# Kernel tuning notes

Measured on AMD Instinct MI355X. Metric: run time of the kernel, lower is better.

Reference implementation:

```python
import jax, jax.numpy as jnp
import numpy as np
from jax import lax

B, C, H, W = 32, 256, 64, 64
MCH = 16   # max(8, 256//16)
KS = 5     # ECA 1D kernel: int((log2(256)+1)/2)=4 -> odd-adjust 5
EPS = 1e-5

def setup_inputs() -> dict:
    key = jax.random.key(0)
    ks = jax.random.split(key, 9)
    return {
        "x": jax.random.normal(ks[0], (B, C, H, W), jnp.float32),
        "w10": jax.random.normal(ks[1], (MCH, C), jnp.float32) * 0.05,   # 1x1 conv C->MCH
        "w11": jax.random.normal(ks[2], (C, MCH), jnp.float32) * 0.05,   # 1x1 conv MCH->C
        "bn_gamma": jax.random.normal(ks[3], (MCH,), jnp.float32) * 0.1 + 1.0,
        "bn_beta": jax.random.normal(ks[4], (MCH,), jnp.float32) * 0.1,
        "bn_mean": jax.random.normal(ks[5], (MCH,), jnp.float32) * 0.1,
        "bn_var": jax.random.uniform(ks[6], (MCH,), jnp.float32, 0.5, 1.5),
        "w20": jax.random.normal(ks[7], (KS,), jnp.float32) * 0.2,       # 1D ECA kernel
        "w21": jax.random.normal(ks[8], (1, 1, 3, 3), jnp.float32) * 0.2,  # spatial 3x3
    }

def reference(x, w10, w11, bn_gamma, bn_beta, bn_mean, bn_var, w20, w21):
    b, c, h, w = x.shape
    # --- channel (ECA) branch: global avg pool -> 1D conv over channel dim ---
    pooled = jnp.mean(x, axis=(2, 3))                      # [b, c]
    f_ch = lax.conv_general_dilated(
        pooled[:, None, :], w20[None, None, :], (1,), 'SAME',
        dimension_numbers=('NCH', 'OIH', 'NCH'))[:, 0, :]   # [b, c]
    f_ch = f_ch[:, :, None, None]                           # [b, c, 1, 1] (no sigmoid, as in source)
    # --- spatial branch: channel mean -> 3x3 conv -> sigmoid ---
    f_sa = jax.nn.sigmoid(lax.conv_general_dilated(
        jnp.mean(x, axis=1, keepdims=True), w21, (1, 1), 'SAME',
        dimension_numbers=('NCHW', 'OIHW', 'NCHW')))        # [b, 1, h, w]
    # --- coordinate branch ---
    x_h = jnp.mean(x, axis=3)                               # [b, c, h]
    x_w = jnp.mean(x, axis=2)                               # [b, c, w]
    cat = jnp.concatenate([x_h, x_w], axis=2)               # [b, c, h+w]
    y = jnp.einsum('mc,bcl->bml', w10, cat)                 # 1x1 conv
    inv = lax.rsqrt(bn_var + EPS) * bn_gamma                # BN (inference)
    y = jax.nn.relu(y * inv[None, :, None] + (bn_beta - bn_mean * inv)[None, :, None])
    yh, yw = y[:, :, :h], y[:, :, h:]
    s_h = jax.nn.sigmoid(jnp.einsum('cm,bmh->bch', w11, yh))[:, :, :, None]  # [b,c,h,1]
    s_w = jax.nn.sigmoid(jnp.einsum('cm,bmw->bcw', w11, yw))[:, :, None, :]  # [b,c,1,w]
    F = f_ch + s_h * s_w + f_sa
    return x * F
```

## Files before the change

### kernel.cpp

```cpp
#include <hip/hip_runtime.h>
#include <hip/hip_bf16.h>

#define NB 32
#define NC 256
#define NH 64
#define NW 64

typedef unsigned short u16;

__device__ int   g_mode;
__device__ float g_cmean[NB * 4096];
__device__ float g_catT[NB * 128 * NC];
__device__ float g_fch[NB * NC];
__device__ float g_fsa[NB * 4096];
__device__ float g_sh[NB * NC * 64];
__device__ float g_sw[NB * NC * 64];

__device__ __forceinline__ float bf2f(unsigned int u) {
    union { unsigned int i; float f; } v; v.i = u << 16; return v.f;
}
__device__ __forceinline__ u16 f2bf(float f) {
    union { float f; unsigned int i; } v; v.f = f;
    unsigned int i = v.i;
    unsigned int r = (i + 0x7fffu + ((i >> 16) & 1u)) >> 16;
    return (u16)r;
}
__device__ __forceinline__ float sigmoidf_(float x) {
    return 1.f / (1.f + expf(-x));
}

__device__ __forceinline__ void loadx8(const void* x, size_t i8, int mode, float* v) {
    if (mode) {
        const uint4 u = ((const uint4*)x)[i8];
        v[0] = bf2f(u.x & 0xffffu); v[1] = bf2f(u.x >> 16);
        v[2] = bf2f(u.y & 0xffffu); v[3] = bf2f(u.y >> 16);
        v[4] = bf2f(u.z & 0xffffu); v[5] = bf2f(u.z >> 16);
        v[6] = bf2f(u.w & 0xffffu); v[7] = bf2f(u.w >> 16);
    } else {
        const float4 a = ((const float4*)x)[i8 * 2];
        const float4 b = ((const float4*)x)[i8 * 2 + 1];
        v[0] = a.x; v[1] = a.y; v[2] = a.z; v[3] = a.w;
        v[4] = b.x; v[5] = b.y; v[6] = b.z; v[7] = b.w;
    }
}
__device__ __forceinline__ float loadw(const void* p, int i, int mode) {
    return mode ? bf2f((unsigned int)((const u16*)p)[i]) : ((const float*)p)[i];
}
__device__ __forceinline__ void store8(void* o, size_t i8, int mode, const float* v) {
    if (mode) {
        uint4 u;
        u.x = (unsigned int)f2bf(v[0]) | ((unsigned int)f2bf(v[1]) << 16);
        u.y = (unsigned int)f2bf(v[2]) | ((unsigned int)f2bf(v[3]) << 16);
        u.z = (unsigned int)f2bf(v[4]) | ((unsigned int)f2bf(v[5]) << 16);
        u.w = (unsigned int)f2bf(v[6]) | ((unsigned int)f2bf(v[7]) << 16);
        ((uint4*)o)[i8] = u;
    } else {
        ((float4*)o)[i8 * 2]     = make_float4(v[0], v[1], v[2], v[3]);
        ((float4*)o)[i8 * 2 + 1] = make_float4(v[4], v[5], v[6], v[7]);
    }
}

__global__ __launch_bounds__(256) void kSniff(const u16* __restrict__ xr) {
    __shared__ int cnt;
    if (threadIdx.x == 0) cnt = 0;
    __syncthreads();
    int local = 0;
#pragma unroll
    for (int i = 0; i < 8; ++i) {
        const u16 w = xr[(threadIdx.x * 8 + i) * 2];
        const unsigned e = (w >> 7) & 0xffu;
        if (w == 0 || (e >= 0x40u && e <= 0x90u)) ++local;
    }
    atomicAdd(&cnt, local);
    __syncthreads();
    if (threadIdx.x == 0) g_mode = (cnt >= 1536) ? 1 : 0;
}

__global__ __launch_bounds__(256) void kZero() {
    const int j = (blockIdx.x * 256 + threadIdx.x) * 4;
    *(float4*)(g_cmean + j) = make_float4(0.f, 0.f, 0.f, 0.f);
}

__global__ __launch_bounds__(256) void kA(const void* __restrict__ x) {
    __shared__ float cmean_lds[4096];
    __shared__ __align__(16) float plane_f[4096];
    __shared__ float rowsum[16 * 64];
    __shared__ float colsum[16 * 64];
    __shared__ float colpart[256];

    const int t  = threadIdx.x;
    const int cg = blockIdx.x;
    const int b  = blockIdx.y;
    const int mode = g_mode;

    for (int j = t; j < 4096; j += 256) cmean_lds[j] = 0.f;
    __syncthreads();

    for (int ch = 0; ch < 16; ++ch) {
        const int c = cg * 16 + ch;
        const size_t plane_i8 = ((size_t)(b * NC + c)) << 9;
#pragma unroll
        for (int i = 0; i < 2; ++i) {
            const int j = i * 2048 + t * 8;
            float v[8];
            loadx8(x, plane_i8 + (j >> 3), mode, v);
            *(float4*)(plane_f + j)     = make_float4(v[0], v[1], v[2], v[3]);
            *(float4*)(plane_f + j + 4) = make_float4(v[4], v[5], v[6], v[7]);
            cmean_lds[j + 0] += v[0]; cmean_lds[j + 1] += v[1];
            cmean_lds[j + 2] += v[2]; cmean_lds[j + 3] += v[3];
            cmean_lds[j + 4] += v[4]; cmean_lds[j + 5] += v[5];
            cmean_lds[j + 6] += v[6]; cmean_lds[j + 7] += v[7];
            float s = ((v[0] + v[1]) + (v[2] + v[3])) + ((v[4] + v[5]) + (v[6] + v[7]));
            s += __shfl_xor(s, 1);
            s += __shfl_xor(s, 2);
            s += __shfl_xor(s, 4);
            if ((t & 7) == 0) rowsum[ch * 64 + (j >> 6)] = s;
        }
        __syncthreads();
        {
            const int col = t & 63, hr = t >> 6;
            float p = 0.f;
#pragma unroll
            for (int hh = 0; hh < 16; ++hh)
                p += plane_f[(hr * 16 + hh) * 64 + col];
            colpart[t] = p;
        }
        __syncthreads();
        if (t < 64)
            colsum[ch * 64 + t] =
                colpart[t] + colpart[64 + t] + colpart[128 + t] + colpart[192 + t];
        __syncthreads();
    }

    const float inv64 = 1.f / 64.f;
    {
        const int lc = t & 15;
#pragma unroll
        for (int r = 0; r < 8; ++r) {
            const int l = r * 16 + (t >> 4);
            const float val =
                (l < 64 ? rowsum[lc * 64 + l] : colsum[lc * 64 + (l - 64)]) * inv64;
            g_catT[((size_t)(b * 128 + l)) * NC + cg * 16 + lc] = val;
        }
    }
    const float invC = 1.f / 256.f;
    for (int j = t; j < 4096; j += 256)
        atomicAdd(&g_cmean[b * 4096 + j], cmean_lds[j] * invC);
}

#define W10_STRIDE 260
__global__ __launch_bounds__(256) void kB(
    const void* __restrict__ w10, const void* __restrict__ w11,
    const void* __restrict__ bn_gamma, const void* __restrict__ bn_beta,
    const void* __restrict__ bn_mean, const void* __restrict__ bn_var,
    const void* __restrict__ w20, const void* __restrict__ w21) {

    __shared__ __align__(16) float un[48 * W10_STRIDE];
    __shared__ float y_lds[16 * 129];
    __shared__ float pooled[260];
    __shared__ float bnA[16], bnB[16], w20f[5], w21f[9];

    const int t = threadIdx.x, b = blockIdx.x;
    const int mode = g_mode;
    float* w10_lds = un;
    float* cat_lds = un + 16 * W10_STRIDE;

    for (int j = t; j < 4096; j += 256)
        w10_lds[(j >> 8) * W10_STRIDE + (j & 255)] = loadw(w10, j, mode);
    if (t < 16) {
        const float inv = rsqrtf(loadw(bn_var, t, mode) + 1e-5f) *
                          loadw(bn_gamma, t, mode);
        bnA[t] = inv;
        bnB[t] = loadw(bn_beta, t, mode) - loadw(bn_mean, t, mode) * inv;
    }
    if (t < 5) w20f[t] = loadw(w20, t, mode);
    if (t < 9) w21f[t] = loadw(w21, t, mode);
    {
        float p = 0.f;
        for (int l = 0; l < 64; ++l) p += g_catT[((size_t)(b * 128 + l)) * NC + t];
        pooled[2 + t] = p * (1.f / 64.f);
    }
    if (t < 2) { pooled[t] = 0.f; pooled[258 + t] = 0.f; }
    __syncthreads();
    {
        float acc = 0.f;
#pragma unroll
        for (int k = 0; k < 5; ++k) acc = fmaf(w20f[k], pooled[t + k], acc);
        g_fch[b * 256 + t] = acc;
    }
    for (int q = 0; q < 4; ++q) {
        __syncthreads();
#pragma unroll
        for (int r = 0; r < 8; ++r) {
            const int idx4 = r * 256 + t;
            const int l = idx4 >> 6;
            const int c = (idx4 & 63) << 2;
            const float4 v =
                *(const float4*)(g_catT + ((size_t)(b * 128 + q * 32 + l)) * NC + c);
            *(float4*)(cat_lds + l * W10_STRIDE + c) = v;
        }
        __syncthreads();
#pragma unroll
        for (int rep = 0; rep < 2; ++rep) {
            const int o = rep * 256 + t;
            const int m = o & 15, li = o >> 4;
            const float4* wr = (const float4*)(w10_lds + m * W10_STRIDE);
            const float4* cr = (const float4*)(cat_lds + li * W10_STRIDE);
            float acc = 0.f;
#pragma unroll 8
            for (int c4 = 0; c4 < 64; ++c4) {
                const float4 a = wr[c4], v = cr[c4];
                acc = fmaf(a.x, v.x, fmaf(a.y, v.y, fmaf(a.z, v.z, fmaf(a.w, v.w, acc))));
            }
            const float yv = fmaxf(fmaf(acc, bnA[m], bnB[m]), 0.f);
            y_lds[m * 129 + q * 32 + li] = yv;
        }
    }
    __syncthreads();
    float* w11f = un;
    float* cm   = un + 4096;
    for (int j = t; j < 4096; j += 256) {
        w11f[j] = loadw(w11, j, mode);
        cm[j]   = g_cmean[b * 4096 + j];
    }
    __syncthreads();
    for (int it = 0; it < 64; ++it) {
        const int c  = it * 4 + (t >> 6);
        const int hw = t & 63;
        const float* wc = w11f + c * 16;
        float ah = 0.f, aw = 0.f;
#pragma unroll
        for (int m = 0; m < 16; ++m) {
            ah = fmaf(wc[m], y_lds[m * 129 + hw], ah);
            aw = fmaf(wc[m], y_lds[m * 129 + 64 + hw], aw);
        }
        g_sh[((size_t)(b * NC + c)) * 64 + hw] = sigmoidf_(ah);
        g_sw[((size_t)(b * NC + c)) * 64 + hw] = sigmoidf_(aw);
    }
    for (int r = 0; r < 16; ++r) {
        const int j = r * 256 + t;
        const int h = j >> 6, w = j & 63;
        float acc = 0.f;
#pragma unroll
        for (int dy = 0; dy < 3; ++dy) {
            const int hy = h + dy - 1;
            if (hy < 0 || hy > 63) continue;
#pragma unroll
            for (int dx = 0; dx < 3; ++dx) {
                const int wx = w + dx - 1;
                if (wx < 0 || wx > 63) continue;
                acc = fmaf(w21f[dy * 3 + dx], cm[hy * 64 + wx], acc);
            }
        }
        g_fsa[b * 4096 + j] = sigmoidf_(acc);
    }
}

__global__ __launch_bounds__(256) void kC(const void* __restrict__ x,
                                          void* __restrict__ out) {
    const unsigned e = blockIdx.x * 256 + threadIdx.x;
    const int w0 = (e & 7) << 3;
    const int h  = (e >> 3) & 63;
    const int c  = (e >> 9) & 255;
    const int b  = e >> 17;
    const int mode = g_mode;

    float v[8];
    loadx8(x, e, mode, v);

    const float fc = g_fch[b * 256 + c];
    const float sh = g_sh[((size_t)(b * NC + c)) * 64 + h];
    const float* swp = g_sw + ((size_t)(b * NC + c)) * 64 + w0;
    const float* fsp = g_fsa + (size_t)b * 4096 + h * 64 + w0;
    const float4 swa = *(const float4*)(swp);
    const float4 swb = *(const float4*)(swp + 4);
    const float4 fsa = *(const float4*)(fsp);
    const float4 fsb = *(const float4*)(fsp + 4);

    float r[8];
    r[0] = v[0] * (fc + sh * swa.x + fsa.x);
    r[1] = v[1] * (fc + sh * swa.y + fsa.y);
    r[2] = v[2] * (fc + sh * swa.z + fsa.z);
    r[3] = v[3] * (fc + sh * swa.w + fsa.w);
    r[4] = v[4] * (fc + sh * swb.x + fsb.x);
    r[5] = v[5] * (fc + sh * swb.y + fsb.y);
    r[6] = v[6] * (fc + sh * swb.z + fsb.z);
    r[7] = v[7] * (fc + sh * swb.w + fsb.w);

    store8(out, e, mode, r);
}

extern "C" void kernel_launch(void* const* d_in, const int* in_sizes, int n_in,
                              void* d_out, int out_size, void* d_ws, size_t ws_size,
                              hipStream_t stream) {
    const void* x        = d_in[0];
    const void* w10      = d_in[1];
    const void* w11      = d_in[2];
    const void* bn_gamma = d_in[3];
    const void* bn_beta  = d_in[4];
    const void* bn_mean  = d_in[5];
    const void* bn_var   = d_in[6];
    const void* w20      = d_in[7];
    const void* w21      = d_in[8];

    kSniff<<<1, 256, 0, stream>>>((const u16*)x);
    kZero<<<(NB * 4096 / 4) / 256, 256, 0, stream>>>();
    kA<<<dim3(16, NB), 256, 0, stream>>>(x);
    kB<<<NB, 256, 0, stream>>>(w10, w11, bn_gamma, bn_beta,
                               bn_mean, bn_var, w20, w21);
    kC<<<(NB * NC * NH * NW / 8) / 256, 256, 0, stream>>>(x, d_out);
}
```

Before: 320.1 us.

## Restructure pooling kernel per-wave and split the coordinate kernel across blocks

In the pooling kernel, each wave now processes 4 channels and keeps column sums in registers, reducing them with shuffles. This removes the per-channel LDS plane staging and three block barriers per channel. Channel-mean partials are packed as bf16 in LDS and written to per-channel-group buffers instead of atomics, so the zeroing kernel can be dropped. The second kernel now runs 4 blocks per batch, splitting the h/w halves, the channel halves and the f_ch/f_sa side work, which adds parallelism. The cost is some duplicated weight loads and a small precision loss in the channel mean from the bf16 partials.

Result: no change. 313.8 us (-2.0%).

```diff
diff --git a/kernel.cpp b/kernel.cpp
--- a/kernel.cpp
+++ b/kernel.cpp
@@ -9,7 +9,7 @@
 typedef unsigned short u16;
 
 __device__ int   g_mode;
-__device__ float g_cmean[NB * 4096];
+__device__ float g_cmeanp[NB * 16 * 4096];
 __device__ float g_catT[NB * 128 * NC];
 __device__ float g_fch[NB * NC];
 __device__ float g_fsa[NB * 4096];
@@ -24,6 +24,9 @@
     unsigned int i = v.i;
     unsigned int r = (i + 0x7fffu + ((i >> 16) & 1u)) >> 16;
     return (u16)r;
+}
+__device__ __forceinline__ unsigned int pack2(float a, float b) {
+    return (unsigned int)f2bf(a) | ((unsigned int)f2bf(b) << 16);
 }
 __device__ __forceinline__ float sigmoidf_(float x) {
     return 1.f / (1.f + expf(-x));
@@ -49,10 +52,10 @@
 __device__ __forceinline__ void store8(void* o, size_t i8, int mode, const float* v) {
     if (mode) {
         uint4 u;
-        u.x = (unsigned int)f2bf(v[0]) | ((unsigned int)f2bf(v[1]) << 16);
-        u.y = (unsigned int)f2bf(v[2]) | ((unsigned int)f2bf(v[3]) << 16);
-        u.z = (unsigned int)f2bf(v[4]) | ((unsigned int)f2bf(v[5]) << 16);
-        u.w = (unsigned int)f2bf(v[6]) | ((unsigned int)f2bf(v[7]) << 16);
+        u.x = pack2(v[0], v[1]);
+        u.y = pack2(v[2], v[3]);
+        u.z = pack2(v[4], v[5]);
+        u.w = pack2(v[6], v[7]);
         ((uint4*)o)[i8] = u;
     } else {
         ((float4*)o)[i8 * 2]     = make_float4(v[0], v[1], v[2], v[3]);
@@ -76,61 +79,74 @@
     if (threadIdx.x == 0) g_mode = (cnt >= 1536) ? 1 : 0;
 }
 
-__global__ __launch_bounds__(256) void kZero() {
-    const int j = (blockIdx.x * 256 + threadIdx.x) * 4;
-    *(float4*)(g_cmean + j) = make_float4(0.f, 0.f, 0.f, 0.f);
-}
-
 __global__ __launch_bounds__(256) void kA(const void* __restrict__ x) {
-    __shared__ float cmean_lds[4096];
-    __shared__ __align__(16) float plane_f[4096];
+    __shared__ unsigned int sliceP[4][2048];
     __shared__ float rowsum[16 * 64];
     __shared__ float colsum[16 * 64];
-    __shared__ float colpart[256];
 
     const int t  = threadIdx.x;
+    const int ln = t & 63, wv = t >> 6;
     const int cg = blockIdx.x;
     const int b  = blockIdx.y;
     const int mode = g_mode;
 
-    for (int j = t; j < 4096; j += 256) cmean_lds[j] = 0.f;
-    __syncthreads();
-
-    for (int ch = 0; ch < 16; ++ch) {
-        const int c = cg * 16 + ch;
-        const size_t plane_i8 = ((size_t)(b * NC + c)) << 9;
-#pragma unroll
-        for (int i = 0; i < 2; ++i) {
-            const int j = i * 2048 + t * 8;
+    float colacc[4][8];
+#pragma unroll
+    for (int cc = 0; cc < 4; ++cc)
+#pragma unroll
+        for (int k = 0; k < 8; ++k) colacc[cc][k] = 0.f;
+
+    const int ch0 = cg * 16 + wv * 4;
+    const size_t i8base = (((size_t)(b * NC + ch0)) << 9) + ln;
+
+    for (int p = 0; p < 8; ++p) {
+        float cme[8];
+#pragma unroll
+        for (int k = 0; k < 8; ++k) cme[k] = 0.f;
+#pragma unroll
+        for (int cc = 0; cc < 4; ++cc) {
             float v[8];
-            loadx8(x, plane_i8 + (j >> 3), mode, v);
-            *(float4*)(plane_f + j)     = make_float4(v[0], v[1], v[2], v[3]);
-            *(float4*)(plane_f + j + 4) = make_float4(v[4], v[5], v[6], v[7]);
-            cmean_lds[j + 0] += v[0]; cmean_lds[j + 1] += v[1];
-            cmean_lds[j + 2] += v[2]; cmean_lds[j + 3] += v[3];
-            cmean_lds[j + 4] += v[4]; cmean_lds[j + 5] += v[5];
-            cmean_lds[j + 6] += v[6]; cmean_lds[j + 7] += v[7];
+            loadx8(x, i8base + (((size_t)cc) << 9) + p * 64, mode, v);
+#pragma unroll
+            for (int k = 0; k < 8; ++k) {
+                cme[k] += v[k];
+                colacc[cc][k] += v[k];
+            }
             float s = ((v[0] + v[1]) + (v[2] + v[3])) + ((v[4] + v[5]) + (v[6] + v[7]));
             s += __shfl_xor(s, 1);
             s += __shfl_xor(s, 2);
             s += __shfl_xor(s, 4);
-            if ((t & 7) == 0) rowsum[ch * 64 + (j >> 6)] = s;
-        }
-        __syncthreads();
-        {
-            const int col = t & 63, hr = t >> 6;
-            float p = 0.f;
-#pragma unroll
-            for (int hh = 0; hh < 16; ++hh)
-                p += plane_f[(hr * 16 + hh) * 64 + col];
-            colpart[t] = p;
-        }
-        __syncthreads();
-        if (t < 64)
-            colsum[ch * 64 + t] =
-                colpart[t] + colpart[64 + t] + colpart[128 + t] + colpart[192 + t];
-        __syncthreads();
-    }
+            if ((ln & 7) == 0)
+                rowsum[(wv * 4 + cc) * 64 + p * 8 + (ln >> 3)] = s;
+        }
+        uint4 pk;
+        pk.x = pack2(cme[0], cme[1]);
+        pk.y = pack2(cme[2], cme[3]);
+        pk.z = pack2(cme[4], cme[5]);
+        pk.w = pack2(cme[6], cme[7]);
+        *(uint4*)&sliceP[wv][p * 256 + ln * 4] = pk;
+    }
+
+#pragma unroll
+    for (int cc = 0; cc < 4; ++cc)
+#pragma unroll
+        for (int k = 0; k < 8; ++k) {
+            float v = colacc[cc][k];
+            v += __shfl_xor(v, 8);
+            v += __shfl_xor(v, 16);
+            v += __shfl_xor(v, 32);
+            colacc[cc][k] = v;
+        }
+    if (ln < 8) {
+#pragma unroll
+        for (int cc = 0; cc < 4; ++cc) {
+            *(float4*)&colsum[(wv * 4 + cc) * 64 + ln * 8] =
+                make_float4(colacc[cc][0], colacc[cc][1], colacc[cc][2], colacc[cc][3]);
+            *(float4*)&colsum[(wv * 4 + cc) * 64 + ln * 8 + 4] =
+                make_float4(colacc[cc][4], colacc[cc][5], colacc[cc][6], colacc[cc][7]);
+        }
+    }
+    __syncthreads();
 
     const float inv64 = 1.f / 64.f;
     {
@@ -143,116 +159,154 @@
             g_catT[((size_t)(b * 128 + l)) * NC + cg * 16 + lc] = val;
         }
     }
-    const float invC = 1.f / 256.f;
-    for (int j = t; j < 4096; j += 256)
-        atomicAdd(&g_cmean[b * 4096 + j], cmean_lds[j] * invC);
-}
-
-#define W10_STRIDE 260
+    {
+        const int u0 = t * 8;
+        float acc[16];
+#pragma unroll
+        for (int k = 0; k < 16; ++k) acc[k] = 0.f;
+#pragma unroll
+        for (int w = 0; w < 4; ++w) {
+            const uint4 qa = *(const uint4*)&sliceP[w][u0];
+            const uint4 qb = *(const uint4*)&sliceP[w][u0 + 4];
+            const unsigned int uu[8] = {qa.x, qa.y, qa.z, qa.w, qb.x, qb.y, qb.z, qb.w};
+#pragma unroll
+            for (int k = 0; k < 8; ++k) {
+                acc[2 * k]     += bf2f(uu[k] & 0xffffu);
+                acc[2 * k + 1] += bf2f(uu[k] >> 16);
+            }
+        }
+        const float invC = 1.f / 256.f;
+        float* dst = g_cmeanp + (((size_t)(b * 16 + cg)) << 12) + t * 16;
+#pragma unroll
+        for (int k4 = 0; k4 < 4; ++k4)
+            *(float4*)(dst + k4 * 4) = make_float4(acc[k4 * 4] * invC,
+                                                   acc[k4 * 4 + 1] * invC,
+                                                   acc[k4 * 4 + 2] * invC,
+                                                   acc[k4 * 4 + 3] * invC);
+    }
+}
+
 __global__ __launch_bounds__(256) void kB(
     const void* __restrict__ w10, const void* __restrict__ w11,
     const void* __restrict__ bn_gamma, const void* __restrict__ bn_beta,
     const void* __restrict__ bn_mean, const void* __restrict__ bn_var,
     const void* __restrict__ w20, const void* __restrict__ w21) {
 
-    __shared__ __align__(16) float un[48 * W10_STRIDE];
-    __shared__ float y_lds[16 * 129];
+    __shared__ float w10_lds[16 * 260];
+    __shared__ float w11_lds[2048];
+    __shared__ float y_lds[16 * 65];
+    __shared__ float cm[4096];
     __shared__ float pooled[260];
-    __shared__ float bnA[16], bnB[16], w20f[5], w21f[9];
-
-    const int t = threadIdx.x, b = blockIdx.x;
+    __shared__ float bnA[16], bnBv[16];
+
+    const int t  = threadIdx.x;
+    const int bx = blockIdx.x;
+    const int half = bx >> 1, csplit = bx & 1;
+    const int b  = blockIdx.y;
     const int mode = g_mode;
-    float* w10_lds = un;
-    float* cat_lds = un + 16 * W10_STRIDE;
 
     for (int j = t; j < 4096; j += 256)
-        w10_lds[(j >> 8) * W10_STRIDE + (j & 255)] = loadw(w10, j, mode);
+        w10_lds[(j >> 8) * 260 + (j & 255)] = loadw(w10, j, mode);
+    for (int j = t; j < 2048; j += 256)
+        w11_lds[j] = loadw(w11, csplit * 2048 + j, mode);
     if (t < 16) {
         const float inv = rsqrtf(loadw(bn_var, t, mode) + 1e-5f) *
                           loadw(bn_gamma, t, mode);
-        bnA[t] = inv;
-        bnB[t] = loadw(bn_beta, t, mode) - loadw(bn_mean, t, mode) * inv;
-    }
-    if (t < 5) w20f[t] = loadw(w20, t, mode);
-    if (t < 9) w21f[t] = loadw(w21, t, mode);
+        bnA[t]  = inv;
+        bnBv[t] = loadw(bn_beta, t, mode) - loadw(bn_mean, t, mode) * inv;
+    }
+    __syncthreads();
+
     {
-        float p = 0.f;
-        for (int l = 0; l < 64; ++l) p += g_catT[((size_t)(b * 128 + l)) * NC + t];
-        pooled[2 + t] = p * (1.f / 64.f);
-    }
-    if (t < 2) { pooled[t] = 0.f; pooled[258 + t] = 0.f; }
-    __syncthreads();
-    {
-        float acc = 0.f;
-#pragma unroll
-        for (int k = 0; k < 5; ++k) acc = fmaf(w20f[k], pooled[t + k], acc);
-        g_fch[b * 256 + t] = acc;
-    }
-    for (int q = 0; q < 4; ++q) {
-        __syncthreads();
-#pragma unroll
-        for (int r = 0; r < 8; ++r) {
-            const int idx4 = r * 256 + t;
-            const int l = idx4 >> 6;
-            const int c = (idx4 & 63) << 2;
-            const float4 v =
-                *(const float4*)(g_catT + ((size_t)(b * 128 + q * 32 + l)) * NC + c);
-            *(float4*)(cat_lds + l * W10_STRIDE + c) = v;
-        }
-        __syncthreads();
-#pragma unroll
-        for (int rep = 0; rep < 2; ++rep) {
-            const int o = rep * 256 + t;
-            const int m = o & 15, li = o >> 4;
-            const float4* wr = (const float4*)(w10_lds + m * W10_STRIDE);
-            const float4* cr = (const float4*)(cat_lds + li * W10_STRIDE);
+        const int m = t & 15, li = t >> 4;
+#pragma unroll
+        for (int rep = 0; rep < 4; ++rep) {
+            const int l = rep * 16 + li;
+            const float4* cr =
+                (const float4*)(g_catT + ((size_t)(b * 128 + half * 64 + l)) * NC);
+            const float4* wr = (const float4*)(w10_lds + m * 260);
             float acc = 0.f;
 #pragma unroll 8
             for (int c4 = 0; c4 < 64; ++c4) {
                 const float4 a = wr[c4], v = cr[c4];
                 acc = fmaf(a.x, v.x, fmaf(a.y, v.y, fmaf(a.z, v.z, fmaf(a.w, v.w, acc))));
             }
-            const float yv = fmaxf(fmaf(acc, bnA[m], bnB[m]), 0.f);
-            y_lds[m * 129 + q * 32 + li] = yv;
-        }
-    }
-    __syncthreads();
-    float* w11f = un;
-    float* cm   = un + 4096;
-    for (int j = t; j < 4096; j += 256) {
-        w11f[j] = loadw(w11, j, mode);
-        cm[j]   = g_cmean[b * 4096 + j];
-    }
-    __syncthreads();
-    for (int it = 0; it < 64; ++it) {
-        const int c  = it * 4 + (t >> 6);
-        const int hw = t & 63;
-        const float* wc = w11f + c * 16;
-        float ah = 0.f, aw = 0.f;
-#pragma unroll
-        for (int m = 0; m < 16; ++m) {
-            ah = fmaf(wc[m], y_lds[m * 129 + hw], ah);
-            aw = fmaf(wc[m], y_lds[m * 129 + 64 + hw], aw);
-        }
-        g_sh[((size_t)(b * NC + c)) * 64 + hw] = sigmoidf_(ah);
-        g_sw[((size_t)(b * NC + c)) * 64 + hw] = sigmoidf_(aw);
-    }
-    for (int r = 0; r < 16; ++r) {
-        const int j = r * 256 + t;
-        const int h = j >> 6, w = j & 63;
+            y_lds[m * 65 + l] = fmaxf(fmaf(acc, bnA[m], bnBv[m]), 0.f);
+        }
+    }
+    __syncthreads();
+
+    {
+        const int h = t & 63, q = t >> 6;
+        float yr[16];
+#pragma unroll
+        for (int mm = 0; mm < 16; ++mm) yr[mm] = y_lds[mm * 65 + h];
+        float* sout = half ? g_sw : g_sh;
+        const size_t sb = ((size_t)b) * NC * 64;
+        for (int ci = 0; ci < 32; ++ci) {
+            const int cl = q * 32 + ci;
+            const float4* wrow = (const float4*)(w11_lds + cl * 16);
+            const float4 w0 = wrow[0], w1 = wrow[1], w2 = wrow[2], w3 = wrow[3];
+            float acc;
+            acc = fmaf(w0.x, yr[0], w0.y * yr[1]);
+            acc = fmaf(w0.z, yr[2], acc); acc = fmaf(w0.w, yr[3], acc);
+            acc = fmaf(w1.x, yr[4], acc); acc = fmaf(w1.y, yr[5], acc);
+            acc = fmaf(w1.z, yr[6], acc); acc = fmaf(w1.w, yr[7], acc);
+            acc = fmaf(w2.x, yr[8], acc); acc = fmaf(w2.y, yr[9], acc);
+            acc = fmaf(w2.z, yr[10], acc); acc = fmaf(w2.w, yr[11], acc);
+            acc = fmaf(w3.x, yr[12], acc); acc = fmaf(w3.y, yr[13], acc);
+            acc = fmaf(w3.z, yr[14], acc); acc = fmaf(w3.w, yr[15], acc);
+            sout[sb + (size_t)(csplit * 128 + cl) * 64 + h] = sigmoidf_(acc);
+        }
+    }
+
+    if (bx == 0) {
+        float p = 0.f;
+        for (int l = 0; l < 64; ++l)
+            p += g_catT[((size_t)(b * 128 + l)) * NC + t];
+        pooled[2 + t] = p * (1.f / 64.f);
+        if (t < 2) { pooled[t] = 0.f; pooled[258 + t] = 0.f; }
+        __syncthreads();
+        float w20f[5];
+#pragma unroll
+        for (int k = 0; k < 5; ++k) w20f[k] = loadw(w20, k, mode);
         float acc = 0.f;
 #pragma unroll
-        for (int dy = 0; dy < 3; ++dy) {
-            const int hy = h + dy - 1;
-            if (hy < 0 || hy > 63) continue;
-#pragma unroll
-            for (int dx = 0; dx < 3; ++dx) {
-                const int wx = w + dx - 1;
-                if (wx < 0 || wx > 63) continue;
-                acc = fmaf(w21f[dy * 3 + dx], cm[hy * 64 + wx], acc);
-            }
-        }
-        g_fsa[b * 4096 + j] = sigmoidf_(acc);
+        for (int k = 0; k < 5; ++k) acc = fmaf(w20f[k], pooled[t + k], acc);
+        g_fch[b * NC + t] = acc;
+    } else if (bx == 1) {
+#pragma unroll
+        for (int it = 0; it < 4; ++it) {
+            const int j = it * 1024 + t * 4;
+            float4 s = make_float4(0.f, 0.f, 0.f, 0.f);
+            for (int gcg = 0; gcg < 16; ++gcg) {
+                const float4 v =
+                    *(const float4*)&g_cmeanp[(((size_t)(b * 16 + gcg)) << 12) + j];
+                s.x += v.x; s.y += v.y; s.z += v.z; s.w += v.w;
+            }
+            *(float4*)&cm[j] = s;
+        }
+        __syncthreads();
+        float w21f[9];
+#pragma unroll
+        for (int k = 0; k < 9; ++k) w21f[k] = loadw(w21, k, mode);
+        for (int r = 0; r < 16; ++r) {
+            const int j = r * 256 + t;
+            const int hh = j >> 6, ww = j & 63;
+            float acc = 0.f;
+#pragma unroll
+            for (int dy = 0; dy < 3; ++dy) {
+                const int hy = hh + dy - 1;
+                if (hy < 0 || hy > 63) continue;
+#pragma unroll
+                for (int dx = 0; dx < 3; ++dx) {
+                    const int wx = ww + dx - 1;
+                    if (wx < 0 || wx > 63) continue;
+                    acc = fmaf(w21f[dy * 3 + dx], cm[hy * 64 + wx], acc);
+                }
+            }
+            g_fsa[b * 4096 + j] = sigmoidf_(acc);
+        }
     }
 }
 
@@ -268,7 +322,7 @@
     float v[8];
     loadx8(x, e, mode, v);
 
-    const float fc = g_fch[b * 256 + c];
+    const float fc = g_fch[b * NC + c];
     const float sh = g_sh[((size_t)(b * NC + c)) * 64 + h];
     const float* swp = g_sw + ((size_t)(b * NC + c)) * 64 + w0;
     const float* fsp = g_fsa + (size_t)b * 4096 + h * 64 + w0;
@@ -304,9 +358,8 @@
     const void* w21      = d_in[8];
 
     kSniff<<<1, 256, 0, stream>>>((const u16*)x);
-    kZero<<<(NB * 4096 / 4) / 256, 256, 0, stream>>>();
     kA<<<dim3(16, NB), 256, 0, stream>>>(x);
-    kB<<<NB, 256, 0, stream>>>(w10, w11, bn_gamma, bn_beta,
-                               bn_mean, bn_var, w20, w21);
+    kB<<<dim3(4, NB), 256, 0, stream>>>(w10, w11, bn_gamma, bn_beta,
+                                        bn_mean, bn_var, w20, w21);
     kC<<<(NB * NC * NH * NW / 8) / 256, 256, 0, stream>>>(x, d_out);
 }
```
